# Optimization experiments

Hardware: AMD Instinct MI355X
Metric: run time of the kernel (lower is better)

## Reference

```python
import jax, jax.numpy as jnp
import numpy as np

MODEL_DIM = 1024
NUM_HEADS = 16
HEAD_DIM = MODEL_DIM // NUM_HEADS
BATCH = 16
KEY_LEN = 4096


def setup_inputs() -> dict:
    key = jax.random.key(0)
    ks = jax.random.split(key, 10)
    u = lambda k, shape: jax.random.uniform(k, shape, jnp.float32, -0.5, 0.5)
    return {
        "hidden_states": jax.random.normal(ks[0], (BATCH, 1, MODEL_DIM), jnp.float32),
        "key_value_states": jax.random.normal(ks[1], (BATCH, KEY_LEN, MODEL_DIM), jnp.float32),
        "Wq": u(ks[2], (MODEL_DIM, MODEL_DIM)), "bq": u(ks[3], (MODEL_DIM,)),
        "Wk": u(ks[4], (MODEL_DIM, MODEL_DIM)), "bk": u(ks[5], (MODEL_DIM,)),
        "Wv": u(ks[6], (MODEL_DIM, MODEL_DIM)), "bv": u(ks[7], (MODEL_DIM,)),
        "Wo": u(ks[8], (MODEL_DIM, MODEL_DIM)), "bo": u(ks[9], (MODEL_DIM,)),
    }


def reference(hidden_states, key_value_states, Wq, bq, Wk, bk, Wv, bv, Wo, bo):
    B, K = key_value_states.shape[0], key_value_states.shape[1]
    H, Dh = NUM_HEADS, HEAD_DIM
    # projections (nn.Linear: x @ W.T + b)
    q = hidden_states @ Wq.T + bq            # [B, 1, H*Dh]
    k = key_value_states @ Wk.T + bk         # [B, K, H*Dh]
    v = key_value_states @ Wv.T + bv         # [B, K, H*Dh]
    # split heads
    q = q.reshape(B, 1, H, Dh).transpose(0, 2, 1, 3)   # [B, H, 1, Dh]
    k = k.reshape(B, K, H, Dh).transpose(0, 2, 1, 3)   # [B, H, K, Dh]
    v = v.reshape(B, K, H, Dh).transpose(0, 2, 1, 3)   # [B, H, K, Dh]
    q = q / jnp.sqrt(jnp.asarray(Dh, q.dtype))
    # scores: [B, H, K] (query_len == 1, squeezed)
    scores = jnp.einsum("bhqd,bhkd->bhqk", q, k)[:, :, 0, :]
    # Hardtanh(min_val=0, max_val=1) gate instead of softmax; dropout p=0
    attn = jnp.clip(scores, 0.0, 1.0)                  # [B, H, K]
    # broadcast-multiply with value, merge heads back
    context = attn[..., None] * v                      # [B, H, K, Dh]
    context = context.transpose(0, 2, 1, 3).reshape(B, K, H * Dh)
    output = context @ Wo.T + bo                       # [B, K, model_dim]
    return output
```

## Files before the change

### kernel.cpp

```cpp
#include <hip/hip_runtime.h>
#include <hip/hip_bf16.h>
#include <stdint.h>

typedef __bf16 bf16x8 __attribute__((ext_vector_type(8)));
typedef __bf16 bf16x4 __attribute__((ext_vector_type(4)));
typedef float  f32x4  __attribute__((ext_vector_type(4)));

#define B_  16
#define KL  4096
#define D_  1024
#define NH  16
#define NROWS (B_*KL)

__device__ __forceinline__ void gload_lds16(const void* g, void* l) {
  __builtin_amdgcn_global_load_lds(
      (__attribute__((address_space(1))) void*)g,
      (__attribute__((address_space(3))) void*)l, 16, 0, 0);
}


__global__ __launch_bounds__(256) void conv_w_kernel(const float* __restrict__ wv,
                                                     const float* __restrict__ wo,
                                                     __bf16* __restrict__ dv,
                                                     __bf16* __restrict__ do_) {
  const bool second = blockIdx.x >= 1024;
  const int i = (second ? blockIdx.x - 1024 : blockIdx.x) * 256 + threadIdx.x;
  const float* s = second ? wo : wv;
  __bf16* d = second ? do_ : dv;
  float4 v = reinterpret_cast<const float4*>(s)[i];
  bf16x4 o;
  o[0] = (__bf16)v.x; o[1] = (__bf16)v.y; o[2] = (__bf16)v.z; o[3] = (__bf16)v.w;
  *reinterpret_cast<bf16x4*>(d + (size_t)i * 4) = o;
}

__global__ __launch_bounds__(256) void wqeff_kernel(const float* __restrict__ hs,
                                                    const float* __restrict__ Wq,
                                                    const float* __restrict__ bq,
                                                    const float* __restrict__ Wk,
                                                    const float* __restrict__ bk,
                                                    __bf16* __restrict__ whi,
                                                    __bf16* __restrict__ wlo,
                                                    float* __restrict__ cb) {
  const int h = blockIdx.x, b = blockIdx.y;
  const int tid = threadIdx.x;
  __shared__ float hsl[D_];
  __shared__ float ql[64];
  {
    float4 v = reinterpret_cast<const float4*>(hs + (size_t)b * D_)[tid];
    hsl[tid * 4] = v.x; hsl[tid * 4 + 1] = v.y;
    hsl[tid * 4 + 2] = v.z; hsl[tid * 4 + 3] = v.w;
  }
  __syncthreads();
  {
    const int d = tid >> 2, seg = tid & 3;
    const float* wr = Wq + (size_t)(h * 64 + d) * D_ + seg * 256;
    const float* xs = hsl + seg * 256;
    float p = 0.f;
    for (int i = 0; i < 256; i += 4) {
      float4 wv4 = *reinterpret_cast<const float4*>(wr + i);
      p += xs[i] * wv4.x + xs[i + 1] * wv4.y + xs[i + 2] * wv4.z + xs[i + 3] * wv4.w;
    }
    p += __shfl_xor(p, 1);
    p += __shfl_xor(p, 2);
    if (seg == 0) ql[d] = (p + bq[h * 64 + d]) * 0.125f;
  }
  __syncthreads();
  float a0 = 0, a1 = 0, a2 = 0, a3 = 0;
  for (int d = 0; d < 64; ++d) {
    float qv = ql[d];
    const float* wr = Wk + (size_t)(h * 64 + d) * D_;
    a0 += qv * wr[tid];
    a1 += qv * wr[tid + 256];
    a2 += qv * wr[tid + 512];
    a3 += qv * wr[tid + 768];
  }
  const size_t base = ((size_t)b * NH + h) * D_;
  float a[4] = {a0, a1, a2, a3};
#pragma unroll
  for (int j = 0; j < 4; ++j) {
    __bf16 hi = (__bf16)a[j];
    whi[base + j * 256 + tid] = hi;
    wlo[base + j * 256 + tid] = (__bf16)(a[j] - (float)hi);
  }
  if (tid < 64) {
    float p = ql[tid] * bk[h * 64 + tid];
    p += __shfl_down(p, 32); p += __shfl_down(p, 16); p += __shfl_down(p, 8);
    p += __shfl_down(p, 4);  p += __shfl_down(p, 2);  p += __shfl_down(p, 1);
    if (tid == 0) cb[b * NH + h] = p;
  }
}

__global__ __launch_bounds__(512) void scores_mfma_kernel(
    const float* __restrict__ kvs,
    const __bf16* __restrict__ whi,
    const __bf16* __restrict__ wlo,
    const float* __restrict__ cb,
    float* __restrict__ attn,
    __bf16* __restrict__ kvd) {
  __shared__ f32x4 part[4][64];
  const int b = blockIdx.y;
  const int tid = threadIdx.x;
  const int lane = tid & 63, wv = tid >> 6;
  const int rg = wv & 3;
  const int kh = wv >> 2;
  const int r16 = lane & 15, kgrp = lane >> 4;
  const int row0 = blockIdx.x * 64 + rg * 16;
  const size_t grow = (size_t)b * KL + row0;
  const int kbase = kh * 512;

  const float* xrow = kvs + (grow + r16) * D_ + kbase + kgrp * 8;
  __bf16*      krow = kvd + (grow + r16) * D_ + kbase + kgrp * 8;
  const __bf16* wh = whi + ((size_t)b * NH + r16) * D_ + kbase + kgrp * 8;
  const __bf16* wl = wlo + ((size_t)b * NH + r16) * D_ + kbase + kgrp * 8;

  f32x4 acc0 = {}, acc1 = {};

#define SPROC(xx0, xx1, kk)                                                     \
  {                                                                             \
    bf16x8 bh = *reinterpret_cast<const bf16x8*>(wh + (kk));                    \
    bf16x8 bl = *reinterpret_cast<const bf16x8*>(wl + (kk));                    \
    float xs[8] = {xx0.x, xx0.y, xx0.z, xx0.w, xx1.x, xx1.y, xx1.z, xx1.w};     \
    bf16x8 hi, lo;                                                              \
    _Pragma("unroll") for (int i = 0; i < 8; ++i) {                             \
      __bf16 h = (__bf16)xs[i];                                                 \
      hi[i] = h;                                                                \
      lo[i] = (__bf16)(xs[i] - (float)h);                                       \
    }                                                                           \
    *reinterpret_cast<bf16x8*>(krow + (kk)) = hi;                               \
    acc0 = __builtin_amdgcn_mfma_f32_16x16x32_bf16(hi, bh, acc0, 0, 0, 0);      \
    acc1 = __builtin_amdgcn_mfma_f32_16x16x32_bf16(hi, bl, acc1, 0, 0, 0);      \
    acc1 = __builtin_amdgcn_mfma_f32_16x16x32_bf16(lo, bh, acc1, 0, 0, 0);      \
  }

  float4 xa0 = *reinterpret_cast<const float4*>(xrow);
  float4 xa1 = *reinterpret_cast<const float4*>(xrow + 4);
  float4 xb0 = *reinterpret_cast<const float4*>(xrow + 32);
  float4 xb1 = *reinterpret_cast<const float4*>(xrow + 36);
  for (int k0 = 0; k0 < 512; k0 += 64) {
    float4 na0, na1, nb0, nb1;
    if (k0 + 64 < 512) {
      na0 = *reinterpret_cast<const float4*>(xrow + k0 + 64);
      na1 = *reinterpret_cast<const float4*>(xrow + k0 + 68);
      nb0 = *reinterpret_cast<const float4*>(xrow + k0 + 96);
      nb1 = *reinterpret_cast<const float4*>(xrow + k0 + 100);
    }
    SPROC(xa0, xa1, k0);
    SPROC(xb0, xb1, k0 + 32);
    xa0 = na0; xa1 = na1; xb0 = nb0; xb1 = nb1;
  }
#undef SPROC

  if (kh == 1) {
    f32x4 s = acc0;
#pragma unroll
    for (int r = 0; r < 4; ++r) s[r] += acc1[r];
    part[rg][lane] = s;
  }
  __syncthreads();
  if (kh == 0) {
    f32x4 p = part[rg][lane];
    const float c = cb[b * NH + r16];
#pragma unroll
    for (int r = 0; r < 4; ++r) {
      const int orow = row0 + kgrp * 4 + r;
      float s = acc0[r] + acc1[r] + p[r] + c;
      attn[((size_t)b * KL + orow) * NH + r16] = fminf(fmaxf(s, 0.f), 1.f);
    }
  }
}

template <bool GATE>
__global__ __launch_bounds__(512, 2) void gemm_nt(const __bf16* __restrict__ A,
                                                  const __bf16* __restrict__ Bt,
                                                  const float* __restrict__ bias,
                                                  const float* __restrict__ gate,
                                                  void* __restrict__ Cp) {
  __shared__ __bf16 As[2][256 * 64];
  __shared__ __bf16 Bs[2][256 * 64];
  const int tid = threadIdx.x;
  const int lane = tid & 63, wid = tid >> 6;
  const int wm = wid >> 2, wn = wid & 3;
  const int r16 = lane & 15, kgrp = lane >> 4;
  const int bswz = (blockIdx.x & 7) * 128 + (blockIdx.x >> 3);
  const int m0 = (bswz >> 2) * 256;
  const int n0 = (bswz & 3) * 256;

  const int srow = lane >> 3;
  const int scol = ((lane & 7) ^ srow) * 8;

  const int sw0 = ((kgrp) ^ (r16 & 7)) * 8;
  const int sw1 = ((4 + kgrp) ^ (r16 & 7)) * 8;

  f32x4 acc[8][4] = {};

#define STAGE_HALF(dstbuf, srcp, base0, h, k0)                                  \
  {                                                                             \
    _Pragma("unroll") for (int j = 0; j < 2; ++j) {                             \
      const int c = (h) * 16 + wid * 2 + j;                                     \
      gload_lds16((srcp) + (size_t)((base0) + c * 8 + srow) * D_ + (k0) + scol, \
                  &(dstbuf)[c * 512]);                                          \
    }                                                                           \
  }

#define LOAD_BV(Bb, sw)                                                         \
  _Pragma("unroll") for (int nh = 0; nh < 2; ++nh)                              \
    _Pragma("unroll") for (int g = 0; g < 2; ++g)                               \
      bv[nh * 2 + g] = *reinterpret_cast<const bf16x8*>(                        \
          &(Bb)[(nh * 128 + wn * 32 + g * 16 + r16) * 64 + (sw)]);

#define LOAD_AV(Ab, mh, sw)                                                     \
  _Pragma("unroll") for (int f = 0; f < 4; ++f)                                 \
    av[f] = *reinterpret_cast<const bf16x8*>(                                   \
        &(Ab)[((mh) * 128 + wm * 64 + f * 16 + r16) * 64 + (sw)]);

#define MFMA_PHASE(mh)                                                          \
  {                                                                             \
    __builtin_amdgcn_s_setprio(1);                                              \
    _Pragma("unroll") for (int f = 0; f < 4; ++f)                               \
      _Pragma("unroll") for (int q = 0; q < 4; ++q)                             \
        acc[(mh) * 4 + f][q] = __builtin_amdgcn_mfma_f32_16x16x32_bf16(         \
            av[f], bv[q], acc[(mh) * 4 + f][q], 0, 0, 0);                       \
    __builtin_amdgcn_s_setprio(0);                                              \
  }

#define WAITLGKM()                                                              \
  asm volatile("s_waitcnt lgkmcnt(0)" ::: "memory");                            \
  __builtin_amdgcn_sched_barrier(0);

  STAGE_HALF(As[0], A,  m0, 0, 0);
  STAGE_HALF(Bs[0], Bt, n0, 0, 0);
  STAGE_HALF(Bs[0], Bt, n0, 1, 0);
  STAGE_HALF(As[0], A,  m0, 1, 0);
  STAGE_HALF(As[1], A,  m0, 0, 64);
  STAGE_HALF(Bs[1], Bt, n0, 0, 64);
  STAGE_HALF(Bs[1], Bt, n0, 1, 64);
  asm volatile("s_waitcnt vmcnt(8)" ::: "memory");
  __builtin_amdgcn_s_barrier();

  const int NT = D_ / 64;
  for (int t = 0; t < NT; ++t) {
    __bf16* Ab = (t & 1) ? As[1] : As[0];
    __bf16* Bb = (t & 1) ? Bs[1] : Bs[0];
    __bf16* An = (t & 1) ? As[0] : As[1];
    const int k1 = (t + 1) * 64;
    const int k2 = (t + 2) * 64;
    const bool pf1 = (t + 1 < NT);
    const bool pf2 = (t + 2 < NT);
    bf16x8 bv[4], av[4];

    LOAD_BV(Bb, sw0);
    LOAD_AV(Ab, 0, sw0);
    if (pf1) STAGE_HALF(An, A, m0, 1, k1);
    __builtin_amdgcn_s_barrier();
    WAITLGKM();
    MFMA_PHASE(0);
    if (pf1) asm volatile("s_waitcnt vmcnt(8)" ::: "memory");
    else     asm volatile("s_waitcnt vmcnt(0)" ::: "memory");
    __builtin_amdgcn_s_barrier();
    LOAD_AV(Ab, 1, sw0);
    __builtin_amdgcn_s_barrier();
    WAITLGKM();
    MFMA_PHASE(1);
    __builtin_amdgcn_s_barrier();
    LOAD_BV(Bb, sw1);
    LOAD_AV(Ab, 0, sw1);
    __builtin_amdgcn_s_barrier();
    WAITLGKM();
    MFMA_PHASE(0);
    __builtin_amdgcn_s_barrier();
    LOAD_AV(Ab, 1, sw1);
    if (pf2) {
      STAGE_HALF(Ab, A,  m0, 0, k2);
      STAGE_HALF(Bb, Bt, n0, 0, k2);
      STAGE_HALF(Bb, Bt, n0, 1, k2);
    }
    __builtin_amdgcn_s_barrier();
    WAITLGKM();
    MFMA_PHASE(1);
    if (pf2)      asm volatile("s_waitcnt vmcnt(8)" ::: "memory");
    else if (pf1) asm volatile("s_waitcnt vmcnt(2)" ::: "memory");
    __builtin_amdgcn_s_barrier();
  }

#pragma unroll
  for (int mh = 0; mh < 2; ++mh) {
#pragma unroll
    for (int f = 0; f < 4; ++f) {
      const int row0 = m0 + mh * 128 + wm * 64 + f * 16 + kgrp * 4;
#pragma unroll
      for (int nh = 0; nh < 2; ++nh) {
#pragma unroll
        for (int g = 0; g < 2; ++g) {
          const int col = n0 + nh * 128 + wn * 32 + g * 16 + r16;
          const float bc = bias[col];
          const int head = col >> 6;
          f32x4 v = acc[mh * 4 + f][nh * 2 + g];
#pragma unroll
          for (int r = 0; r < 4; ++r) {
            const int row = row0 + r;
            if constexpr (GATE) {
              float gg = gate[(size_t)row * NH + head];
              ((__bf16*)Cp)[(size_t)row * D_ + col] = (__bf16)((v[r] + bc) * gg);
            } else {
              ((float*)Cp)[(size_t)row * D_ + col] = v[r] + bc;
            }
          }
        }
      }
    }
  }
#undef STAGE_HALF
#undef LOAD_BV
#undef LOAD_AV
#undef MFMA_PHASE
#undef WAITLGKM
}

extern "C" void kernel_launch(void* const* d_in, const int* in_sizes, int n_in,
                              void* d_out, int out_size, void* d_ws, size_t ws_size,
                              hipStream_t stream) {
  const float* hs  = (const float*)d_in[0];
  const float* kvs = (const float*)d_in[1];
  const float* Wq  = (const float*)d_in[2];
  const float* bq  = (const float*)d_in[3];
  const float* Wk  = (const float*)d_in[4];
  const float* bk  = (const float*)d_in[5];
  const float* Wv  = (const float*)d_in[6];
  const float* bv  = (const float*)d_in[7];
  const float* Wo  = (const float*)d_in[8];
  const float* bo  = (const float*)d_in[9];
  float* out = (float*)d_out;

  char* w = (char*)d_ws;
  __bf16* ctx  = (__bf16*)w;  w += (size_t)NROWS * D_ * 2;
  float*  attn = (float*)w;   w += (size_t)NROWS * NH * 4;
  __bf16* WvB  = (__bf16*)w;  w += (size_t)D_ * D_ * 2;
  __bf16* WoB  = (__bf16*)w;  w += (size_t)D_ * D_ * 2;
  __bf16* whi  = (__bf16*)w;  w += (size_t)B_ * NH * D_ * 2;
  __bf16* wlo  = (__bf16*)w;  w += (size_t)B_ * NH * D_ * 2;
  float*  cbuf = (float*)w;   w += B_ * NH * 4;

  __bf16* kvsB = (__bf16*)d_out;

  conv_w_kernel<<<2048, 256, 0, stream>>>(Wv, Wo, WvB, WoB);
  wqeff_kernel<<<dim3(NH, B_), 256, 0, stream>>>(hs, Wq, bq, Wk, bk, whi, wlo, cbuf);
  scores_mfma_kernel<<<dim3(KL / 64, B_), 512, 0, stream>>>(kvs, whi, wlo, cbuf, attn, kvsB);
  gemm_nt<true ><<<1024, 512, 0, stream>>>(kvsB, WvB, bv, attn, ctx);
  gemm_nt<false><<<1024, 512, 0, stream>>>(ctx, WoB, bo, (const float*)nullptr, (void*)out);
}
```

Before: 483.0 us.

## Restructure GEMM main loop into quadrant phases with spread-out global prefetch

The bf16 GEMM main loop is reordered so each phase computes one 128x128 output quadrant over the full 64-wide K slice. A fragments for both K halves and two sets of B fragments stay in registers. Global-to-LDS prefetches for the tile two steps ahead are now spread across the four phases instead of being issued in one burst, and the vmcnt waits are adjusted to match. The explicit lgkmcnt waits and scheduling barriers are dropped, so the compiler now places LDS waits. Fragment register use roughly doubles, which risks spills or scheduling slack at two blocks per CU.

```diff
diff --git a/kernel.cpp b/kernel.cpp
--- a/kernel.cpp
+++ b/kernel.cpp
@@ -170,11 +170,11 @@
 }
 
 template <bool GATE>
-__global__ __launch_bounds__(512, 2) void gemm_nt(const __bf16* __restrict__ A,
-                                                  const __bf16* __restrict__ Bt,
-                                                  const float* __restrict__ bias,
-                                                  const float* __restrict__ gate,
-                                                  void* __restrict__ Cp) {
+__global__ __launch_bounds__(512, 2) void gemm_q(const __bf16* __restrict__ A,
+                                                 const __bf16* __restrict__ Bt,
+                                                 const float* __restrict__ bias,
+                                                 const float* __restrict__ gate,
+                                                 void* __restrict__ Cp) {
   __shared__ __bf16 As[2][256 * 64];
   __shared__ __bf16 Bs[2][256 * 64];
   const int tid = threadIdx.x;
@@ -202,30 +202,30 @@
     }                                                                           \
   }
 
-#define LOAD_BV(Bb, sw)                                                         \
-  _Pragma("unroll") for (int nh = 0; nh < 2; ++nh)                              \
+#define LOAD_AVQ(Ab, mh)                                                        \
+  _Pragma("unroll") for (int kk = 0; kk < 2; ++kk)                              \
+    _Pragma("unroll") for (int f = 0; f < 4; ++f)                               \
+      av[kk * 4 + f] = *reinterpret_cast<const bf16x8*>(                        \
+          &(Ab)[((mh) * 128 + wm * 64 + f * 16 + r16) * 64 + (kk ? sw1 : sw0)]);
+
+#define LOAD_BVQ(dst, Bb, nh)                                                   \
+  _Pragma("unroll") for (int kk = 0; kk < 2; ++kk)                              \
     _Pragma("unroll") for (int g = 0; g < 2; ++g)                               \
-      bv[nh * 2 + g] = *reinterpret_cast<const bf16x8*>(                        \
-          &(Bb)[(nh * 128 + wn * 32 + g * 16 + r16) * 64 + (sw)]);
-
-#define LOAD_AV(Ab, mh, sw)                                                     \
-  _Pragma("unroll") for (int f = 0; f < 4; ++f)                                 \
-    av[f] = *reinterpret_cast<const bf16x8*>(                                   \
-        &(Ab)[((mh) * 128 + wm * 64 + f * 16 + r16) * 64 + (sw)]);
-
-#define MFMA_PHASE(mh)                                                          \
+      dst[kk * 2 + g] = *reinterpret_cast<const bf16x8*>(                       \
+          &(Bb)[((nh) * 128 + wn * 32 + g * 16 + r16) * 64 + (kk ? sw1 : sw0)]);
+
+#define MFMA_Q(mh, nh, bvx)                                                     \
   {                                                                             \
     __builtin_amdgcn_s_setprio(1);                                              \
-    _Pragma("unroll") for (int f = 0; f < 4; ++f)                               \
-      _Pragma("unroll") for (int q = 0; q < 4; ++q)                             \
-        acc[(mh) * 4 + f][q] = __builtin_amdgcn_mfma_f32_16x16x32_bf16(         \
-            av[f], bv[q], acc[(mh) * 4 + f][q], 0, 0, 0);                       \
+    _Pragma("unroll") for (int kk = 0; kk < 2; ++kk)                            \
+      _Pragma("unroll") for (int f = 0; f < 4; ++f)                             \
+        _Pragma("unroll") for (int g = 0; g < 2; ++g)                           \
+          acc[(mh) * 4 + f][(nh) * 2 + g] =                                     \
+              __builtin_amdgcn_mfma_f32_16x16x32_bf16(                          \
+                  av[kk * 4 + f], bvx[kk * 2 + g],                              \
+                  acc[(mh) * 4 + f][(nh) * 2 + g], 0, 0, 0);                    \
     __builtin_amdgcn_s_setprio(0);                                              \
   }
-
-#define WAITLGKM()                                                              \
-  asm volatile("s_waitcnt lgkmcnt(0)" ::: "memory");                            \
-  __builtin_amdgcn_sched_barrier(0);
 
   STAGE_HALF(As[0], A,  m0, 0, 0);
   STAGE_HALF(Bs[0], Bt, n0, 0, 0);
@@ -234,7 +234,7 @@
   STAGE_HALF(As[1], A,  m0, 0, 64);
   STAGE_HALF(Bs[1], Bt, n0, 0, 64);
   STAGE_HALF(Bs[1], Bt, n0, 1, 64);
-  asm volatile("s_waitcnt vmcnt(8)" ::: "memory");
+  asm volatile("s_waitcnt vmcnt(6)" ::: "memory");
   __builtin_amdgcn_s_barrier();
 
   const int NT = D_ / 64;
@@ -246,39 +246,29 @@
     const int k2 = (t + 2) * 64;
     const bool pf1 = (t + 1 < NT);
     const bool pf2 = (t + 2 < NT);
-    bf16x8 bv[4], av[4];
-
-    LOAD_BV(Bb, sw0);
-    LOAD_AV(Ab, 0, sw0);
+    bf16x8 av[8], bv0[4], bv1[4];
+
+    LOAD_AVQ(Ab, 0);
+    LOAD_BVQ(bv0, Bb, 0);
     if (pf1) STAGE_HALF(An, A, m0, 1, k1);
     __builtin_amdgcn_s_barrier();
-    WAITLGKM();
-    MFMA_PHASE(0);
-    if (pf1) asm volatile("s_waitcnt vmcnt(8)" ::: "memory");
-    else     asm volatile("s_waitcnt vmcnt(0)" ::: "memory");
-    __builtin_amdgcn_s_barrier();
-    LOAD_AV(Ab, 1, sw0);
-    __builtin_amdgcn_s_barrier();
-    WAITLGKM();
-    MFMA_PHASE(1);
-    __builtin_amdgcn_s_barrier();
-    LOAD_BV(Bb, sw1);
-    LOAD_AV(Ab, 0, sw1);
-    __builtin_amdgcn_s_barrier();
-    WAITLGKM();
-    MFMA_PHASE(0);
-    __builtin_amdgcn_s_barrier();
-    LOAD_AV(Ab, 1, sw1);
-    if (pf2) {
-      STAGE_HALF(Ab, A,  m0, 0, k2);
-      STAGE_HALF(Bb, Bt, n0, 0, k2);
-      STAGE_HALF(Bb, Bt, n0, 1, k2);
-    }
-    __builtin_amdgcn_s_barrier();
-    WAITLGKM();
-    MFMA_PHASE(1);
-    if (pf2)      asm volatile("s_waitcnt vmcnt(8)" ::: "memory");
-    else if (pf1) asm volatile("s_waitcnt vmcnt(2)" ::: "memory");
+    MFMA_Q(0, 0, bv0);
+    __builtin_amdgcn_s_barrier();
+    LOAD_BVQ(bv1, Bb, 1);
+    if (pf2) STAGE_HALF(Ab, A, m0, 0, k2);
+    __builtin_amdgcn_s_barrier();
+    MFMA_Q(0, 1, bv1);
+    __builtin_amdgcn_s_barrier();
+    LOAD_AVQ(Ab, 1);
+    if (pf2) STAGE_HALF(Bb, Bt, n0, 0, k2);
+    __builtin_amdgcn_s_barrier();
+    MFMA_Q(1, 0, bv0);
+    __builtin_amdgcn_s_barrier();
+    if (pf2) STAGE_HALF(Bb, Bt, n0, 1, k2);
+    __builtin_amdgcn_s_barrier();
+    MFMA_Q(1, 1, bv1);
+    if (pf2)      asm volatile("s_waitcnt vmcnt(6)" ::: "memory");
+    else if (pf1) asm volatile("s_waitcnt vmcnt(0)" ::: "memory");
     __builtin_amdgcn_s_barrier();
   }
 
@@ -310,10 +300,9 @@
     }
   }
 #undef STAGE_HALF
-#undef LOAD_BV
-#undef LOAD_AV
-#undef MFMA_PHASE
-#undef WAITLGKM
+#undef LOAD_AVQ
+#undef LOAD_BVQ
+#undef MFMA_Q
 }
 
 extern "C" void kernel_launch(void* const* d_in, const int* in_sizes, int n_in,
@@ -345,6 +334,6 @@
   conv_w_kernel<<<2048, 256, 0, stream>>>(Wv, Wo, WvB, WoB);
   wqeff_kernel<<<dim3(NH, B_), 256, 0, stream>>>(hs, Wq, bq, Wk, bk, whi, wlo, cbuf);
   scores_mfma_kernel<<<dim3(KL / 64, B_), 512, 0, stream>>>(kvs, whi, wlo, cbuf, attn, kvsB);
-  gemm_nt<true ><<<1024, 512, 0, stream>>>(kvsB, WvB, bv, attn, ctx);
-  gemm_nt<false><<<1024, 512, 0, stream>>>(ctx, WoB, bo, (const float*)nullptr, (void*)out);
-}
+  gemm_q<true ><<<1024, 512, 0, stream>>>(kvsB, WvB, bv, attn, ctx);
+  gemm_q<false><<<1024, 512, 0, stream>>>(ctx, WoB, bo, (const float*)nullptr, (void*)out);
+}
```

After: 434.8 us. -10.0%, faster.
